# Optimization experiments

Measured on AMD Instinct MI355X. Metric: run time of the kernel, lower is better.

## Reference

```python
import jax, jax.numpy as jnp
import numpy as np

L, N, E, H, D, F = 2048, 2, 1024, 16, 64, 4096  # seq, batch, embed, heads, head_dim, ffn
EPS = 1e-5


def _ln(x, w, b):
    m = jnp.mean(x, axis=-1, keepdims=True)
    v = jnp.mean(jnp.square(x - m), axis=-1, keepdims=True)
    return (x - m) * jax.lax.rsqrt(v + EPS) * w + b


def setup_inputs() -> dict:
    key = jax.random.key(0)
    ks = jax.random.split(key, 16)
    s = 0.02
    f32 = jnp.float32
    return {
        "x": jax.random.normal(ks[0], (L, N, E), f32),
        "ln1_w": jnp.ones((E,), f32),
        "ln1_b": jnp.zeros((E,), f32),
        "wq": jax.random.normal(ks[1], (H * D, E), f32) * s,
        "bq": jnp.zeros((H * D,), f32),
        "wk": jax.random.normal(ks[2], (H * D, E), f32) * s,
        "bk": jnp.zeros((H * D,), f32),
        "wv": jax.random.normal(ks[3], (H * D, E), f32) * s,
        "bv": jnp.zeros((H * D,), f32),
        "wout": jax.random.normal(ks[4], (E, H * D), f32) * s,
        "bout": jnp.zeros((E,), f32),
        "ln2_w": jnp.ones((E,), f32),
        "ln2_b": jnp.zeros((E,), f32),
        "fc1_w": jax.random.normal(ks[5], (F, E), f32) * s,
        "fc1_b": jnp.zeros((F,), f32),
        "fc2_w": jax.random.normal(ks[6], (E, F), f32) * s,
        "fc2_b": jnp.zeros((E,), f32),
    }


def reference(x, ln1_w, ln1_b, wq, bq, wk, bk, wv, bv, wout, bout,
              ln2_w, ln2_b, fc1_w, fc1_b, fc2_w, fc2_b):
    scale = D ** (-0.5)
    residual = x
    h = _ln(x, ln1_w, ln1_b)                      # (L,N,E)
    q = (h @ wq.T + bq).reshape(L, N, H, D) * scale
    k = (h @ wk.T + bk).reshape(L, N, H, D)
    v = (h @ wv.T + bv).reshape(L, N, H, D)
    attn = jnp.einsum('qnhd,knhd->nhqk', q, k)    # (N,H,L,L) full score matrix
    causal = jnp.tril(jnp.ones((L, L), bool))
    attn = jnp.where(causal[None, None], attn, jnp.float32(-10000.0))
    p = jax.nn.softmax(attn, axis=-1)
    o = jnp.einsum('nhqk,knhd->qnhd', p, v).reshape(L, N, H * D)
    o = o @ wout.T + bout
    x = o + residual
    residual = x
    h = _ln(x, ln2_w, ln2_b)
    h = jax.nn.gelu(h @ fc1_w.T + fc1_b, approximate=False)
    h = h @ fc2_w.T + fc2_b
    return h + residual
```

## Files before the change

kernel.cpp:

```cpp
#include <hip/hip_runtime.h>
#include <hip/hip_bf16.h>
#include <math.h>

using bf16 = __hip_bfloat16;
typedef __bf16 bf16x8 __attribute__((ext_vector_type(8)));
typedef short  short4v __attribute__((ext_vector_type(4)));
typedef float  f32x4  __attribute__((ext_vector_type(4)));

static constexpr int Lq = 2048, Nb = 2, E = 1024, Hh = 16, Dd = 64, Ff = 4096;
static constexpr int MT = Lq * Nb;
static constexpr int QKVLD = 3 * E;
static constexpr int LDL = 2 * QKVLD;

__device__ __forceinline__ void async_lds16(const void* g, void* l) {
  __builtin_amdgcn_global_load_lds(
      (const __attribute__((address_space(1))) void*)g,
      (__attribute__((address_space(3))) void*)l, 16, 0, 0);
}
__device__ __forceinline__ bf16x8 ld8(const bf16* p) { return *(const bf16x8*)p; }
__device__ __forceinline__ short bfbits(float x) {
  bf16 t = __float2bfloat16(x);
  return *(short*)&t;
}

__global__ __launch_bounds__(256) void cvt_all_kernel(
    const float* __restrict__ wq, const float* __restrict__ wk,
    const float* __restrict__ wv, const float* __restrict__ wout,
    const float* __restrict__ fc1w, const float* __restrict__ fc2w,
    bf16* __restrict__ wqkvb, bf16* __restrict__ woutb,
    bf16* __restrict__ f1wb, bf16* __restrict__ f2wb) {
  const int i = blockIdx.x * 256 + threadIdx.x;
  const float* src;
  bf16* dst;
  size_t off;
  if (i < 786432) {
    const int r = i >> 18;
    off = (size_t)(i & 262143);
    src = (r == 0) ? wq : (r == 1) ? wk : wv;
    dst = wqkvb + (size_t)r * (E * E);
  } else if (i < 1048576) {
    off = (size_t)(i - 786432); src = wout; dst = woutb;
  } else if (i < 2097152) {
    off = (size_t)(i - 1048576); src = fc1w; dst = f1wb;
  } else {
    off = (size_t)(i - 2097152); src = fc2w; dst = f2wb;
  }
  float4 v = ((const float4*)src)[off];
  bf16 o4[4] = {__float2bfloat16(v.x), __float2bfloat16(v.y),
                __float2bfloat16(v.z), __float2bfloat16(v.w)};
  *(uint2*)(dst + 4 * off) = *(uint2*)o4;
}

template <int EPI>
__global__ __launch_bounds__(256) void gemm_bt(
    const bf16* __restrict__ A, const bf16* __restrict__ W,
    const float* __restrict__ b1, const float* __restrict__ b2,
    const float* __restrict__ b3, int Klen, int Kstride, int Nld,
    float qscale, int scut, const float* __restrict__ res,
    bf16* __restrict__ outb, float* __restrict__ outf) {
  __shared__ __align__(16) bf16 As[128 * 32];
  __shared__ __align__(16) bf16 Bs[128 * 32];
  const int tid = threadIdx.x;
  const int w = tid >> 6, lane = tid & 63;
  const int quad = lane >> 4, l16 = lane & 15;
  const int wm = (w >> 1) * 64, wn = (w & 1) * 64;
  const int m0 = blockIdx.y * 128, n0 = blockIdx.x * 128;
  const int koff = blockIdx.z * Klen;

  f32x4 acc[4][4];
#pragma unroll
  for (int i = 0; i < 4; i++)
#pragma unroll
    for (int j = 0; j < 4; j++)
#pragma unroll
      for (int r = 0; r < 4; r++) acc[i][j][r] = 0.f;

  const int c0 = w * 64 + lane;
  const int c1 = c0 + 256;
  const size_t arow0 = (size_t)(m0 + (c0 >> 2)), arow1 = (size_t)(m0 + (c1 >> 2));
  const size_t brow0 = (size_t)(n0 + (c0 >> 2)), brow1 = (size_t)(n0 + (c1 >> 2));
  const int col0 = (c0 & 3) * 8, col1 = (c1 & 3) * 8;
  bf16* ldsA0 = &As[(w * 64) * 8];
  bf16* ldsA1 = &As[(256 + w * 64) * 8];
  bf16* ldsB0 = &Bs[(w * 64) * 8];
  bf16* ldsB1 = &Bs[(256 + w * 64) * 8];

  const int nk = Klen >> 5;
  for (int kt = 0; kt < nk; ++kt) {
    const int k0 = koff + kt * 32;
    async_lds16(A + arow0 * Kstride + k0 + col0, ldsA0);
    async_lds16(A + arow1 * Kstride + k0 + col1, ldsA1);
    async_lds16(W + brow0 * Kstride + k0 + col0, ldsB0);
    async_lds16(W + brow1 * Kstride + k0 + col1, ldsB1);
    __syncthreads();
    bf16x8 a[4], b[4];
#pragma unroll
    for (int i = 0; i < 4; i++) {
      a[i] = ld8(&As[(wm + i * 16 + l16) * 32 + quad * 8]);
      b[i] = ld8(&Bs[(wn + i * 16 + l16) * 32 + quad * 8]);
    }
#pragma unroll
    for (int i = 0; i < 4; i++)
#pragma unroll
      for (int j = 0; j < 4; j++)
        acc[i][j] = __builtin_amdgcn_mfma_f32_16x16x32_bf16(a[i], b[j], acc[i][j], 0, 0, 0);
    __syncthreads();
  }

  const size_t zoff = (EPI == 3) ? (size_t)blockIdx.z * ((size_t)MT * E) : 0;
#pragma unroll
  for (int i = 0; i < 4; i++) {
    const int mrow = m0 + wm + i * 16 + quad * 4;
#pragma unroll
    for (int j = 0; j < 4; j++) {
      const int ncol = n0 + wn + j * 16 + l16;
      float bv = 0.f;
      if constexpr (EPI != 3) {
        if (b3 != nullptr) {
          bv = (ncol < 1024) ? b1[ncol]
               : (ncol < 2048) ? b2[ncol - 1024] : b3[ncol - 2048];
        } else {
          bv = b1[ncol];
        }
      }
      const float sc = (ncol < scut) ? qscale : 1.0f;
#pragma unroll
      for (int r = 0; r < 4; r++) {
        const size_t idx = (size_t)(mrow + r) * Nld + ncol;
        float v = (acc[i][j][r] + bv) * sc;
        if constexpr (EPI == 0) {
          outb[idx] = __float2bfloat16(v);
        } else if constexpr (EPI == 1) {
          outf[idx] = v + res[idx];
        } else if constexpr (EPI == 2) {
          v = 0.5f * v * (1.f + erff(v * 0.70710678118f));
          outb[idx] = __float2bfloat16(v);
        } else {
          outb[zoff + idx] = __float2bfloat16(v);
        }
      }
    }
  }
}

__global__ __launch_bounds__(256) void reduce2_kernel(
    const bf16* __restrict__ P, const float* __restrict__ bias,
    const float* __restrict__ res, float* __restrict__ out) {
  const int i = blockIdx.x * 256 + threadIdx.x;
  const size_t e0 = (size_t)i * 4;
  const int col = (int)(e0 & (E - 1));
  uint2 u0 = *(const uint2*)(P + e0);
  uint2 u1 = *(const uint2*)(P + (size_t)MT * E + e0);
  const bf16* p0 = (const bf16*)&u0;
  const bf16* p1 = (const bf16*)&u1;
  float4 b = *(const float4*)(bias + col);
  float4 r = *(const float4*)(res + e0);
  float4 o;
  o.x = (float)p0[0] + (float)p1[0] + b.x + r.x;
  o.y = (float)p0[1] + (float)p1[1] + b.y + r.y;
  o.z = (float)p0[2] + (float)p1[2] + b.z + r.z;
  o.w = (float)p0[3] + (float)p1[3] + b.w + r.w;
  *(float4*)(out + e0) = o;
}

__global__ __launch_bounds__(256) void ln_kernel(
    const float* __restrict__ x, const float* __restrict__ wgt,
    const float* __restrict__ bia, bf16* __restrict__ out) {
  const int t = blockIdx.x, tid = threadIdx.x;
  const size_t base = (size_t)t * E;
  float v4[4], s = 0.f, ss = 0.f;
#pragma unroll
  for (int i = 0; i < 4; i++) {
    float v = x[base + i * 256 + tid];
    v4[i] = v; s += v; ss += v * v;
  }
  for (int off = 32; off > 0; off >>= 1) {
    s += __shfl_down(s, off, 64);
    ss += __shfl_down(ss, off, 64);
  }
  __shared__ float rs[4], rss[4], mv[2];
  const int w = tid >> 6;
  if ((tid & 63) == 0) { rs[w] = s; rss[w] = ss; }
  __syncthreads();
  if (tid == 0) {
    float S = rs[0] + rs[1] + rs[2] + rs[3];
    float SS = rss[0] + rss[1] + rss[2] + rss[3];
    float mean = S * (1.f / E);
    float var = SS * (1.f / E) - mean * mean;
    mv[0] = mean; mv[1] = rsqrtf(var + 1e-5f);
  }
  __syncthreads();
  const float mean = mv[0], rstd = mv[1];
#pragma unroll
  for (int i = 0; i < 4; i++) {
    const int e = i * 256 + tid;
    float r = (v4[i] - mean) * rstd * wgt[e] + bia[e];
    out[base + e] = __float2bfloat16(r);
  }
}

__global__ __launch_bounds__(256) void attn_kernel(
    const bf16* __restrict__ QKV, bf16* __restrict__ O) {
  constexpr int LDT = 72;
  __shared__ __align__(16) bf16 Vt[2][64 * LDT];
  const int tid = threadIdx.x;
  const int w = tid >> 6, lane = tid & 63, quad = lane >> 4, l16 = lane & 15;
  const int pid = blockIdx.x;
  const int hh = blockIdx.y;
  const int n = hh >> 4, h = hh & 15;
  const int hb = n * QKVLD + h * Dd;
  const bf16* Qp = QKV + hb;
  const bf16* Kp = QKV + hb + E;
  const bf16* Vp = QKV + hb + 2 * E;

  const int vrow0 = tid >> 3, vd0 = (tid & 7) * 8;
  const int vrow1 = (tid + 256) >> 3, vd1 = (tid & 7) * 8;

  for (int half = 0; half < 2; ++half) {
    const int qt = (half == 0) ? (31 - pid) : pid;
    __syncthreads();

    const int ql = qt * 64 + w * 16 + l16;
    const bf16x8 aq0 = ld8(Qp + (size_t)ql * LDL + quad * 8);
    const bf16x8 aq1 = ld8(Qp + (size_t)ql * LDL + 32 + quad * 8);

    f32x4 o_acc[4];
#pragma unroll
    for (int d = 0; d < 4; d++)
#pragma unroll
      for (int r = 0; r < 4; r++) o_acc[d][r] = 0.f;
    float m_run = -1e30f, l_run = 0.f;

    bf16x8 kc[4][2];
    uint4 vc0, vc1;
#pragma unroll
    for (int ks = 0; ks < 4; ks++)
#pragma unroll
      for (int c = 0; c < 2; c++)
        kc[ks][c] = ld8(Kp + (size_t)(ks * 16 + l16) * LDL + c * 32 + quad * 8);
    vc0 = *(const uint4*)(Vp + (size_t)vrow0 * LDL + vd0);
    vc1 = *(const uint4*)(Vp + (size_t)vrow1 * LDL + vd1);

    for (int kt = 0; kt <= qt; ++kt) {
      bf16* vb = Vt[kt & 1];
      {
        const bf16* t0 = (const bf16*)&vc0;
        const bf16* t1 = (const bf16*)&vc1;
#pragma unroll
        for (int i = 0; i < 8; i++) vb[(vd0 + i) * LDT + vrow0] = t0[i];
#pragma unroll
        for (int i = 0; i < 8; i++) vb[(vd1 + i) * LDT + vrow1] = t1[i];
      }
      __syncthreads();

      f32x4 s[4];
#pragma unroll
      for (int ks = 0; ks < 4; ks++) {
#pragma unroll
        for (int r = 0; r < 4; r++) s[ks][r] = 0.f;
        s[ks] = __builtin_amdgcn_mfma_f32_16x16x32_bf16(kc[ks][0], aq0, s[ks], 0, 0, 0);
        s[ks] = __builtin_amdgcn_mfma_f32_16x16x32_bf16(kc[ks][1], aq1, s[ks], 0, 0, 0);
      }

      if (kt < qt) {
        const size_t kb = (size_t)(kt + 1) * 64;
#pragma unroll
        for (int ks = 0; ks < 4; ks++)
#pragma unroll
          for (int c = 0; c < 2; c++)
            kc[ks][c] = ld8(Kp + (kb + ks * 16 + l16) * LDL + c * 32 + quad * 8);
        vc0 = *(const uint4*)(Vp + (kb + vrow0) * LDL + vd0);
        vc1 = *(const uint4*)(Vp + (kb + vrow1) * LDL + vd1);
      }

      if (kt == qt) {
#pragma unroll
        for (int ks = 0; ks < 4; ks++) {
#pragma unroll
          for (int r = 0; r < 4; r++) {
            const int kg = kt * 64 + ks * 16 + quad * 4 + r;
            if (kg > ql) s[ks][r] = -10000.0f;
          }
        }
      }

      float tmax = s[0][0];
#pragma unroll
      for (int ks = 0; ks < 4; ks++)
#pragma unroll
        for (int r = 0; r < 4; r++) tmax = fmaxf(tmax, s[ks][r]);
      tmax = fmaxf(tmax, __shfl_xor(tmax, 16, 64));
      tmax = fmaxf(tmax, __shfl_xor(tmax, 32, 64));
      const float mnew = fmaxf(m_run, tmax);
      const float alpha = __expf(m_run - mnew);
      m_run = mnew;
      float rsum = 0.f;
      short4v pf[4];
#pragma unroll
      for (int ks = 0; ks < 4; ks++) {
#pragma unroll
        for (int r = 0; r < 4; r++) {
          const float pv = __expf(s[ks][r] - mnew);
          rsum += pv;
          pf[ks][r] = bfbits(pv);
        }
      }
      rsum += __shfl_xor(rsum, 16, 64);
      rsum += __shfl_xor(rsum, 32, 64);
      l_run = l_run * alpha + rsum;
#pragma unroll
      for (int d = 0; d < 4; d++)
#pragma unroll
        for (int r = 0; r < 4; r++) o_acc[d][r] *= alpha;

#pragma unroll
      for (int d = 0; d < 4; d++) {
#pragma unroll
        for (int ks = 0; ks < 4; ks++) {
          const short4v av =
              *(const short4v*)&vb[(d * 16 + l16) * LDT + ks * 16 + quad * 4];
          o_acc[d] = __builtin_amdgcn_mfma_f32_16x16x16bf16_1k(av, pf[ks], o_acc[d], 0, 0, 0);
        }
      }
    }

    const float inv_l = 1.f / fmaxf(l_run, 1e-20f);
    const size_t obase = (size_t)ql * (Nb * E) + (size_t)n * E + h * Dd;
#pragma unroll
    for (int d = 0; d < 4; d++)
#pragma unroll
      for (int r = 0; r < 4; r++)
        O[obase + d * 16 + quad * 4 + r] = __float2bfloat16(o_acc[d][r] * inv_l);
  }
}

extern "C" void kernel_launch(void* const* d_in, const int* in_sizes, int n_in,
                              void* d_out, int out_size, void* d_ws, size_t ws_size,
                              hipStream_t stream) {
  const float* x    = (const float*)d_in[0];
  const float* ln1w = (const float*)d_in[1];
  const float* ln1b = (const float*)d_in[2];
  const float* wq   = (const float*)d_in[3];
  const float* bq   = (const float*)d_in[4];
  const float* wk   = (const float*)d_in[5];
  const float* bk   = (const float*)d_in[6];
  const float* wv   = (const float*)d_in[7];
  const float* bv   = (const float*)d_in[8];
  const float* wout = (const float*)d_in[9];
  const float* bout = (const float*)d_in[10];
  const float* ln2w = (const float*)d_in[11];
  const float* ln2b = (const float*)d_in[12];
  const float* fc1w = (const float*)d_in[13];
  const float* fc1b = (const float*)d_in[14];
  const float* fc2w = (const float*)d_in[15];
  const float* fc2b = (const float*)d_in[16];

  char* ws = (char*)d_ws;
  bf16* wqkvb = (bf16*)(ws);
  bf16* woutb = (bf16*)(ws + ((size_t)6 << 20));
  bf16* f1wb  = (bf16*)(ws + ((size_t)8 << 20));
  bf16* P01   = (bf16*)(ws);
  bf16* f2wb  = (bf16*)(ws + ((size_t)16 << 20));
  bf16* h1    = (bf16*)(ws + ((size_t)24 << 20));
  bf16* qkv   = (bf16*)(ws + ((size_t)32 << 20));
  bf16* o     = (bf16*)(ws + ((size_t)56 << 20));
  float* x1   = (float*)(ws + ((size_t)64 << 20));
  bf16* f1    = (bf16*)(ws + ((size_t)32 << 20));
  bf16* h2    = h1;
  float* outp = (float*)d_out;

  cvt_all_kernel<<<12288, 256, 0, stream>>>(wq, wk, wv, wout, fc1w, fc2w,
                                            wqkvb, woutb, f1wb, f2wb);

  ln_kernel<<<MT, 256, 0, stream>>>(x, ln1w, ln1b, h1);

  dim3 gQKV(QKVLD / 128, MT / 128);
  dim3 gE(E / 128, MT / 128);
  dim3 gF(Ff / 128, MT / 128);
  dim3 gFC2(E / 128, MT / 128, 2);

  gemm_bt<0><<<gQKV, 256, 0, stream>>>(h1, wqkvb, bq, bk, bv, E, E, QKVLD,
                                       0.125f, 1024, nullptr, qkv, nullptr);

  attn_kernel<<<dim3(16, Nb * Hh), 256, 0, stream>>>(qkv, o);

  gemm_bt<1><<<gE, 256, 0, stream>>>(o, woutb, bout, nullptr, nullptr, E, E, E,
                                     1.f, 0, x, nullptr, x1);
  ln_kernel<<<MT, 256, 0, stream>>>(x1, ln2w, ln2b, h2);
  gemm_bt<2><<<gF, 256, 0, stream>>>(h2, f1wb, fc1b, nullptr, nullptr, E, E, Ff,
                                     1.f, 0, nullptr, f1, nullptr);
  gemm_bt<3><<<gFC2, 256, 0, stream>>>(f1, f2wb, nullptr, nullptr, nullptr,
                                       Ff / 2, Ff, E, 1.f, 0, nullptr, P01, nullptr);
  reduce2_kernel<<<MT * E / 4 / 256, 256, 0, stream>>>(P01, fc2b, x1, outp);
}
```

Measured before the change: 428.5 us.

## Write V transposed from QKV GEMM, drop LDS staging in attention, split-K out-proj

The QKV GEMM epilogue now writes Q/K into a 2048-wide buffer and V directly in a per-head transposed [d][L] layout. With that, the attention kernel can read V fragments straight from global memory instead of transposing through LDS with barriers. The attention kernel also runs both causal halves concurrently as 512-thread blocks, with 8 waves split across two query tiles. The output projection switches to split-K with a bf16 partial buffer plus the existing reduce kernel, which adds bias and residual. The costs are scattered 2-byte transposed stores in the GEMM epilogue, uncached global V loads without prefetch, and extra bf16 rounding of the out-proj partials.

```diff
diff --git a/kernel.cpp b/kernel.cpp
--- a/kernel.cpp
+++ b/kernel.cpp
@@ -9,8 +9,8 @@
 
 static constexpr int Lq = 2048, Nb = 2, E = 1024, Hh = 16, Dd = 64, Ff = 4096;
 static constexpr int MT = Lq * Nb;
-static constexpr int QKVLD = 3 * E;
-static constexpr int LDL = 2 * QKVLD;
+static constexpr int QKLD = 2 * E;
+static constexpr int LDL = 2 * QKLD;
 
 __device__ __forceinline__ void async_lds16(const void* g, void* l) {
   __builtin_amdgcn_global_load_lds(
@@ -56,8 +56,8 @@
     const bf16* __restrict__ A, const bf16* __restrict__ W,
     const float* __restrict__ b1, const float* __restrict__ b2,
     const float* __restrict__ b3, int Klen, int Kstride, int Nld,
-    float qscale, int scut, const float* __restrict__ res,
-    bf16* __restrict__ outb, float* __restrict__ outf) {
+    float qscale, int scut, bf16* __restrict__ outb,
+    bf16* __restrict__ outv) {
   __shared__ __align__(16) bf16 As[128 * 32];
   __shared__ __align__(16) bf16 Bs[128 * 32];
   const int tid = threadIdx.x;
@@ -126,17 +126,20 @@
       const float sc = (ncol < scut) ? qscale : 1.0f;
 #pragma unroll
       for (int r = 0; r < 4; r++) {
-        const size_t idx = (size_t)(mrow + r) * Nld + ncol;
         float v = (acc[i][j][r] + bv) * sc;
-        if constexpr (EPI == 0) {
-          outb[idx] = __float2bfloat16(v);
-        } else if constexpr (EPI == 1) {
-          outf[idx] = v + res[idx];
-        } else if constexpr (EPI == 2) {
+        if constexpr (EPI == 2) {
           v = 0.5f * v * (1.f + erff(v * 0.70710678118f));
-          outb[idx] = __float2bfloat16(v);
+          outb[(size_t)(mrow + r) * Nld + ncol] = __float2bfloat16(v);
+        } else if constexpr (EPI == 3) {
+          outb[zoff + (size_t)(mrow + r) * Nld + ncol] = __float2bfloat16(v);
         } else {
-          outb[zoff + idx] = __float2bfloat16(v);
+          if (ncol < 2048) {
+            outb[(size_t)(mrow + r) * 2048 + ncol] = __float2bfloat16(v);
+          } else {
+            const int h = (ncol - 2048) >> 6, d = ncol & 63;
+            const int tok = mrow + r, n = tok & 1, l = tok >> 1;
+            outv[(size_t)((n * 16 + h) * 64 + d) * Lq + l] = __float2bfloat16(v);
+          }
         }
       }
     }
@@ -199,139 +202,109 @@
   }
 }
 
-__global__ __launch_bounds__(256) void attn_kernel(
-    const bf16* __restrict__ QKV, bf16* __restrict__ O) {
-  constexpr int LDT = 72;
-  __shared__ __align__(16) bf16 Vt[2][64 * LDT];
+__global__ __launch_bounds__(512) void attn_kernel(
+    const bf16* __restrict__ QK, const bf16* __restrict__ VT,
+    bf16* __restrict__ O) {
   const int tid = threadIdx.x;
   const int w = tid >> 6, lane = tid & 63, quad = lane >> 4, l16 = lane & 15;
   const int pid = blockIdx.x;
   const int hh = blockIdx.y;
   const int n = hh >> 4, h = hh & 15;
-  const int hb = n * QKVLD + h * Dd;
-  const bf16* Qp = QKV + hb;
-  const bf16* Kp = QKV + hb + E;
-  const bf16* Vp = QKV + hb + 2 * E;
-
-  const int vrow0 = tid >> 3, vd0 = (tid & 7) * 8;
-  const int vrow1 = (tid + 256) >> 3, vd1 = (tid & 7) * 8;
-
-  for (int half = 0; half < 2; ++half) {
-    const int qt = (half == 0) ? (31 - pid) : pid;
-    __syncthreads();
-
-    const int ql = qt * 64 + w * 16 + l16;
-    const bf16x8 aq0 = ld8(Qp + (size_t)ql * LDL + quad * 8);
-    const bf16x8 aq1 = ld8(Qp + (size_t)ql * LDL + 32 + quad * 8);
-
-    f32x4 o_acc[4];
+  const int qt = (w < 4) ? (31 - pid) : pid;
+  const int wr = (w & 3) * 16;
+
+  const bf16* Qp = QK + n * QKLD + h * Dd;
+  const bf16* Kp = Qp + E;
+  const bf16* Vp = VT + (size_t)hh * 64 * Lq;
+
+  const int ql = qt * 64 + wr + l16;
+  const bf16x8 aq0 = ld8(Qp + (size_t)ql * LDL + quad * 8);
+  const bf16x8 aq1 = ld8(Qp + (size_t)ql * LDL + 32 + quad * 8);
+
+  f32x4 o_acc[4];
+#pragma unroll
+  for (int d = 0; d < 4; d++)
+#pragma unroll
+    for (int r = 0; r < 4; r++) o_acc[d][r] = 0.f;
+  float m_run = -1e30f, l_run = 0.f;
+
+  for (int kt = 0; kt <= qt; ++kt) {
+    const size_t kb = (size_t)kt * 64;
+
+    bf16x8 kc[4][2];
+#pragma unroll
+    for (int ks = 0; ks < 4; ks++)
+#pragma unroll
+      for (int c = 0; c < 2; c++)
+        kc[ks][c] = ld8(Kp + (kb + ks * 16 + l16) * LDL + c * 32 + quad * 8);
+
+    f32x4 s[4];
+#pragma unroll
+    for (int ks = 0; ks < 4; ks++) {
+#pragma unroll
+      for (int r = 0; r < 4; r++) s[ks][r] = 0.f;
+      s[ks] = __builtin_amdgcn_mfma_f32_16x16x32_bf16(kc[ks][0], aq0, s[ks], 0, 0, 0);
+      s[ks] = __builtin_amdgcn_mfma_f32_16x16x32_bf16(kc[ks][1], aq1, s[ks], 0, 0, 0);
+    }
+
+    if (kt == qt) {
+#pragma unroll
+      for (int ks = 0; ks < 4; ks++) {
+#pragma unroll
+        for (int r = 0; r < 4; r++) {
+          const int kg = kt * 64 + ks * 16 + quad * 4 + r;
+          if (kg > ql) s[ks][r] = -10000.0f;
+        }
+      }
+    }
+
+    float tmax = s[0][0];
+#pragma unroll
+    for (int ks = 0; ks < 4; ks++)
+#pragma unroll
+      for (int r = 0; r < 4; r++) tmax = fmaxf(tmax, s[ks][r]);
+    tmax = fmaxf(tmax, __shfl_xor(tmax, 16, 64));
+    tmax = fmaxf(tmax, __shfl_xor(tmax, 32, 64));
+    const float mnew = fmaxf(m_run, tmax);
+    const float alpha = __expf(m_run - mnew);
+    m_run = mnew;
+    float rsum = 0.f;
+    short4v pf[4];
+#pragma unroll
+    for (int ks = 0; ks < 4; ks++) {
+#pragma unroll
+      for (int r = 0; r < 4; r++) {
+        const float pv = __expf(s[ks][r] - mnew);
+        rsum += pv;
+        pf[ks][r] = bfbits(pv);
+      }
+    }
+    rsum += __shfl_xor(rsum, 16, 64);
+    rsum += __shfl_xor(rsum, 32, 64);
+    l_run = l_run * alpha + rsum;
 #pragma unroll
     for (int d = 0; d < 4; d++)
 #pragma unroll
-      for (int r = 0; r < 4; r++) o_acc[d][r] = 0.f;
-    float m_run = -1e30f, l_run = 0.f;
-
-    bf16x8 kc[4][2];
-    uint4 vc0, vc1;
-#pragma unroll
-    for (int ks = 0; ks < 4; ks++)
-#pragma unroll
-      for (int c = 0; c < 2; c++)
-        kc[ks][c] = ld8(Kp + (size_t)(ks * 16 + l16) * LDL + c * 32 + quad * 8);
-    vc0 = *(const uint4*)(Vp + (size_t)vrow0 * LDL + vd0);
-    vc1 = *(const uint4*)(Vp + (size_t)vrow1 * LDL + vd1);
-
-    for (int kt = 0; kt <= qt; ++kt) {
-      bf16* vb = Vt[kt & 1];
-      {
-        const bf16* t0 = (const bf16*)&vc0;
-        const bf16* t1 = (const bf16*)&vc1;
-#pragma unroll
-        for (int i = 0; i < 8; i++) vb[(vd0 + i) * LDT + vrow0] = t0[i];
-#pragma unroll
-        for (int i = 0; i < 8; i++) vb[(vd1 + i) * LDT + vrow1] = t1[i];
-      }
-      __syncthreads();
-
-      f32x4 s[4];
+      for (int r = 0; r < 4; r++) o_acc[d][r] *= alpha;
+
+#pragma unroll
+    for (int d = 0; d < 4; d++) {
 #pragma unroll
       for (int ks = 0; ks < 4; ks++) {
-#pragma unroll
-        for (int r = 0; r < 4; r++) s[ks][r] = 0.f;
-        s[ks] = __builtin_amdgcn_mfma_f32_16x16x32_bf16(kc[ks][0], aq0, s[ks], 0, 0, 0);
-        s[ks] = __builtin_amdgcn_mfma_f32_16x16x32_bf16(kc[ks][1], aq1, s[ks], 0, 0, 0);
-      }
-
-      if (kt < qt) {
-        const size_t kb = (size_t)(kt + 1) * 64;
-#pragma unroll
-        for (int ks = 0; ks < 4; ks++)
-#pragma unroll
-          for (int c = 0; c < 2; c++)
-            kc[ks][c] = ld8(Kp + (kb + ks * 16 + l16) * LDL + c * 32 + quad * 8);
-        vc0 = *(const uint4*)(Vp + (kb + vrow0) * LDL + vd0);
-        vc1 = *(const uint4*)(Vp + (kb + vrow1) * LDL + vd1);
-      }
-
-      if (kt == qt) {
-#pragma unroll
-        for (int ks = 0; ks < 4; ks++) {
-#pragma unroll
-          for (int r = 0; r < 4; r++) {
-            const int kg = kt * 64 + ks * 16 + quad * 4 + r;
-            if (kg > ql) s[ks][r] = -10000.0f;
-          }
-        }
-      }
-
-      float tmax = s[0][0];
-#pragma unroll
-      for (int ks = 0; ks < 4; ks++)
-#pragma unroll
-        for (int r = 0; r < 4; r++) tmax = fmaxf(tmax, s[ks][r]);
-      tmax = fmaxf(tmax, __shfl_xor(tmax, 16, 64));
-      tmax = fmaxf(tmax, __shfl_xor(tmax, 32, 64));
-      const float mnew = fmaxf(m_run, tmax);
-      const float alpha = __expf(m_run - mnew);
-      m_run = mnew;
-      float rsum = 0.f;
-      short4v pf[4];
-#pragma unroll
-      for (int ks = 0; ks < 4; ks++) {
-#pragma unroll
-        for (int r = 0; r < 4; r++) {
-          const float pv = __expf(s[ks][r] - mnew);
-          rsum += pv;
-          pf[ks][r] = bfbits(pv);
-        }
-      }
-      rsum += __shfl_xor(rsum, 16, 64);
-      rsum += __shfl_xor(rsum, 32, 64);
-      l_run = l_run * alpha + rsum;
-#pragma unroll
-      for (int d = 0; d < 4; d++)
-#pragma unroll
-        for (int r = 0; r < 4; r++) o_acc[d][r] *= alpha;
-
-#pragma unroll
-      for (int d = 0; d < 4; d++) {
-#pragma unroll
-        for (int ks = 0; ks < 4; ks++) {
-          const short4v av =
-              *(const short4v*)&vb[(d * 16 + l16) * LDT + ks * 16 + quad * 4];
-          o_acc[d] = __builtin_amdgcn_mfma_f32_16x16x16bf16_1k(av, pf[ks], o_acc[d], 0, 0, 0);
-        }
-      }
-    }
-
-    const float inv_l = 1.f / fmaxf(l_run, 1e-20f);
-    const size_t obase = (size_t)ql * (Nb * E) + (size_t)n * E + h * Dd;
-#pragma unroll
-    for (int d = 0; d < 4; d++)
-#pragma unroll
-      for (int r = 0; r < 4; r++)
-        O[obase + d * 16 + quad * 4 + r] = __float2bfloat16(o_acc[d][r] * inv_l);
-  }
+        const short4v av =
+            *(const short4v*)(Vp + (size_t)(d * 16 + l16) * Lq + kb + ks * 16 + quad * 4);
+        o_acc[d] = __builtin_amdgcn_mfma_f32_16x16x16bf16_1k(av, pf[ks], o_acc[d], 0, 0, 0);
+      }
+    }
+  }
+
+  const float inv_l = 1.f / fmaxf(l_run, 1e-20f);
+  const size_t obase = (size_t)ql * (Nb * E) + (size_t)n * E + h * Dd;
+#pragma unroll
+  for (int d = 0; d < 4; d++)
+#pragma unroll
+    for (int r = 0; r < 4; r++)
+      O[obase + d * 16 + quad * 4 + r] = __float2bfloat16(o_acc[d][r] * inv_l);
 }
 
 extern "C" void kernel_launch(void* const* d_in, const int* in_sizes, int n_in,
@@ -359,12 +332,14 @@
   bf16* wqkvb = (bf16*)(ws);
   bf16* woutb = (bf16*)(ws + ((size_t)6 << 20));
   bf16* f1wb  = (bf16*)(ws + ((size_t)8 << 20));
-  bf16* P01   = (bf16*)(ws);
   bf16* f2wb  = (bf16*)(ws + ((size_t)16 << 20));
   bf16* h1    = (bf16*)(ws + ((size_t)24 << 20));
-  bf16* qkv   = (bf16*)(ws + ((size_t)32 << 20));
+  bf16* qk    = (bf16*)(ws + ((size_t)32 << 20));
+  bf16* vtg   = (bf16*)(ws + ((size_t)48 << 20));
   bf16* o     = (bf16*)(ws + ((size_t)56 << 20));
   float* x1   = (float*)(ws + ((size_t)64 << 20));
+  bf16* Pout  = (bf16*)(ws + ((size_t)32 << 20));
+  bf16* P01   = (bf16*)(ws);
   bf16* f1    = (bf16*)(ws + ((size_t)32 << 20));
   bf16* h2    = h1;
   float* outp = (float*)d_out;
@@ -374,22 +349,25 @@
 
   ln_kernel<<<MT, 256, 0, stream>>>(x, ln1w, ln1b, h1);
 
-  dim3 gQKV(QKVLD / 128, MT / 128);
-  dim3 gE(E / 128, MT / 128);
+  dim3 gQKV(3 * E / 128, MT / 128);
+  dim3 gE2(E / 128, MT / 128, 2);
   dim3 gF(Ff / 128, MT / 128);
-  dim3 gFC2(E / 128, MT / 128, 2);
-
-  gemm_bt<0><<<gQKV, 256, 0, stream>>>(h1, wqkvb, bq, bk, bv, E, E, QKVLD,
-                                       0.125f, 1024, nullptr, qkv, nullptr);
-
-  attn_kernel<<<dim3(16, Nb * Hh), 256, 0, stream>>>(qkv, o);
-
-  gemm_bt<1><<<gE, 256, 0, stream>>>(o, woutb, bout, nullptr, nullptr, E, E, E,
-                                     1.f, 0, x, nullptr, x1);
+
+  gemm_bt<4><<<gQKV, 256, 0, stream>>>(h1, wqkvb, bq, bk, bv, E, E, 2048,
+                                       0.125f, 1024, qk, vtg);
+
+  attn_kernel<<<dim3(16, Nb * Hh), 512, 0, stream>>>(qk, vtg, o);
+
+  gemm_bt<3><<<gE2, 256, 0, stream>>>(o, woutb, nullptr, nullptr, nullptr,
+                                      E / 2, E, E, 1.f, 0, Pout, nullptr);
+  reduce2_kernel<<<MT * E / 1024, 256, 0, stream>>>(Pout, bout, x, x1);
+
   ln_kernel<<<MT, 256, 0, stream>>>(x1, ln2w, ln2b, h2);
+
   gemm_bt<2><<<gF, 256, 0, stream>>>(h2, f1wb, fc1b, nullptr, nullptr, E, E, Ff,
-                                     1.f, 0, nullptr, f1, nullptr);
-  gemm_bt<3><<<gFC2, 256, 0, stream>>>(f1, f2wb, nullptr, nullptr, nullptr,
-                                       Ff / 2, Ff, E, 1.f, 0, nullptr, P01, nullptr);
-  reduce2_kernel<<<MT * E / 4 / 256, 256, 0, stream>>>(P01, fc2b, x1, outp);
-}
+                                     1.f, 0, f1, nullptr);
+
+  gemm_bt<3><<<gE2, 256, 0, stream>>>(f1, f2wb, nullptr, nullptr, nullptr,
+                                      Ff / 2, Ff, E, 1.f, 0, P01, nullptr);
+  reduce2_kernel<<<MT * E / 1024, 256, 0, stream>>>(P01, fc2b, x1, outp);
+}
```

Result: slower. 523.0 us (+22.0%).
